# Optimization experiments

Hardware: AMD Instinct MI355X
Metric: run time of the kernel (lower is better)

The kernel has to match this reference:

```python
import jax, jax.numpy as jnp
import numpy as np

N_NODES = 100000


def gcn_conv(x, src, dst, W, b, n):
    # PyG GCNConv: add self-loops, symmetric deg^-1/2 normalization,
    # linear transform, gather->scatter-add aggregation, + bias.
    loop = jnp.arange(n, dtype=src.dtype)
    s = jnp.concatenate([src, loop])
    d = jnp.concatenate([dst, loop])
    deg = jax.ops.segment_sum(jnp.ones_like(d, dtype=x.dtype), d, num_segments=n)
    dinv = jnp.where(deg > 0, jax.lax.rsqrt(deg), jnp.zeros_like(deg))
    norm = dinv[s] * dinv[d]            # [E+N]
    h = x @ W                            # [N, out] (transform before propagate)
    msg = h[s] * norm[:, None]           # gather + scale
    out = jax.ops.segment_sum(msg, d, num_segments=n)  # scatter-add to dst
    return out + b


def setup_inputs() -> dict:
    key = jax.random.key(0)
    k = jax.random.split(key, 6)
    n, e, c_in, hid, c_out = N_NODES, 2500000, 5, 32, 1
    x = jax.random.normal(k[0], (n, c_in), dtype=jnp.float32)
    edge_index = jax.random.randint(k[1], (2, e), 0, n, dtype=jnp.int64)
    # Glorot-style init for GCN weights, zero bias (PyG default)
    W1 = jax.random.normal(k[2], (c_in, hid), dtype=jnp.float32) * (1.0 / np.sqrt(c_in))
    b1 = jnp.zeros((hid,), dtype=jnp.float32)
    W2 = jax.random.normal(k[3], (hid, c_out), dtype=jnp.float32) * (1.0 / np.sqrt(hid))
    b2 = jnp.zeros((c_out,), dtype=jnp.float32)
    return {"x": x, "edge_index": edge_index, "W1": W1, "b1": b1, "W2": W2, "b2": b2}


def reference(x, edge_index, W1, b1, W2, b2):
    n = x.shape[0]
    src, dst = edge_index[0], edge_index[1]
    h = jax.nn.relu(gcn_conv(x, src, dst, W1, b1, n))
    # dropout p=0.3 is identity at inference (training=False)
    return jax.nn.sigmoid(gcn_conv(h, src, dst, W2, b2, n))
```

## Files before the change

kernel.cpp:

```cpp
#include <hip/hip_runtime.h>
#include <math.h>


#define NB_SHIFT  8
#define BNODES    256
#define NBK       512
#define CAP       8192
#define CAP_SHIFT 13
#define CHUNK     8192
#define PBLK      512

__global__ void k_init(int* __restrict__ bcur) {
    int b = threadIdx.x;
    if (b < NBK) bcur[b] = b << CAP_SHIFT;
}

__global__ __launch_bounds__(PBLK) void k_part(const int* __restrict__ src,
                                               const int* __restrict__ dst, int E,
                                               int* __restrict__ bcur,
                                               int* __restrict__ pairs) {
    __shared__ int sp[CHUNK];
    __shared__ unsigned short sb[CHUNK];
    __shared__ int cnt[NBK], ofs[NBK], cur[NBK], gbase[NBK];
    int tid = threadIdx.x;
    int base = blockIdx.x * CHUNK;
    int m = min(CHUNK, E - base);

    if (tid < NBK) cnt[tid] = 0;
    __syncthreads();
    for (int i = tid; i < m; i += PBLK)
        atomicAdd(&cnt[dst[base + i] >> NB_SHIFT], 1);
    __syncthreads();
    int v = cnt[tid];
    ofs[tid] = v;
    __syncthreads();
    for (int off = 1; off < NBK; off <<= 1) {
        int u = (tid >= off) ? ofs[tid - off] : 0;
        __syncthreads();
        ofs[tid] += u;
        __syncthreads();
    }
    int pre = ofs[tid] - v;
    ofs[tid] = pre;
    cur[tid] = pre;
    gbase[tid] = v ? atomicAdd(&bcur[tid], v) : 0;
    __syncthreads();
    for (int i = tid; i < m; i += PBLK) {
        int s = src[base + i], d = dst[base + i];
        int b = d >> NB_SHIFT;
        int p = atomicAdd(&cur[b], 1);
        sp[p] = ((d & (BNODES - 1)) << 24) | s;
        sb[p] = (unsigned short)b;
    }
    __syncthreads();
    for (int i = tid; i < m; i += PBLK) {
        int b = sb[i];
        pairs[gbase[b] + (i - ofs[b])] = sp[i];
    }
}

__global__ __launch_bounds__(512) void k_sortb(int* __restrict__ pairs,
                                               const int* __restrict__ bcur,
                                               const float* __restrict__ x,
                                               float* __restrict__ dinv,
                                               float* __restrict__ xs,
                                               int* __restrict__ nofs,
                                               int* __restrict__ deg, int n) {
    __shared__ int stage[CAP];
    __shared__ int stage2[CAP];
    __shared__ int cnt[BNODES], cur[BNODES], scn[BNODES];
    int tid = threadIdx.x;
    int b = blockIdx.x;
    int base = b << CAP_SHIFT;
    int len = min(bcur[b] - base, CAP);

    for (int i = tid; i < len; i += 512) stage[i] = pairs[base + i];
    if (tid < BNODES) cnt[tid] = 0;
    __syncthreads();
    for (int i = tid; i < len; i += 512)
        atomicAdd(&cnt[((unsigned)stage[i]) >> 24], 1);
    __syncthreads();
    int v = (tid < BNODES) ? cnt[tid] : 0;
    if (tid < BNODES) scn[tid] = v;
    __syncthreads();
    for (int off = 1; off < BNODES; off <<= 1) {
        int u = (tid < BNODES && tid >= off) ? scn[tid - off] : 0;
        __syncthreads();
        if (tid < BNODES) scn[tid] += u;
        __syncthreads();
    }
    if (tid < BNODES) {
        int pos = scn[tid] - v;
        cur[tid] = pos;
        int node = (b << NB_SHIFT) + tid;
        if (node < n) {
            nofs[node] = base + pos;
            deg[node] = v;
            float di = rsqrtf((float)v + 1.0f);
            dinv[node] = di;
            const float* xr = x + (size_t)node * 5;
            float* xo = xs + ((size_t)node << 3);
#pragma unroll
            for (int k = 0; k < 5; ++k) xo[k] = xr[k] * di;
        }
    }
    __syncthreads();
    for (int i = tid; i < len; i += 512) {
        int vv = stage[i];
        int p = atomicAdd(&cur[((unsigned)vv) >> 24], 1);
        stage2[p] = vv & 0x00FFFFFF;
    }
    __syncthreads();
    for (int i = tid; i < len; i += 512) pairs[base + i] = stage2[i];
}

__global__ __launch_bounds__(256) void k_agg1(const int* __restrict__ pairs,
                                              const int* __restrict__ nofs,
                                              const int* __restrict__ deg,
                                              const float* __restrict__ xs,
                                              const float* __restrict__ dinv,
                                              const float* __restrict__ W1,
                                              const float* __restrict__ b1,
                                              const float* __restrict__ W2,
                                              float* __restrict__ h2s, int n) {
    __shared__ float w1[160], bb1[32], w2[32];
    int tid = threadIdx.x;
    if (tid < 160) w1[tid] = W1[tid];
    else if (tid < 192) bb1[tid - 160] = b1[tid - 160];
    else if (tid < 224) w2[tid - 192] = W2[tid - 192];
    __syncthreads();
    int node = blockIdx.x * 128 + (tid >> 1);
    int half = tid & 1;
    if (node >= n) return;
    int beg = nofs[node], dg = deg[node];
    float a0 = 0.f, a1 = 0.f, a2 = 0.f, a3 = 0.f, a4 = 0.f;
    if (!half) {
        const float* xo = xs + ((size_t)node << 3);
        a0 = xo[0]; a1 = xo[1]; a2 = xo[2]; a3 = xo[3]; a4 = xo[4];
    }
    for (int e = beg + half; e < beg + dg; e += 2) {
        int s = pairs[e];
        const float* xr = xs + ((size_t)s << 3);
        float4 q = *(const float4*)xr;
        float q4 = xr[4];
        a0 += q.x; a1 += q.y; a2 += q.z; a3 += q.w; a4 += q4;
    }
    a0 += __shfl_xor(a0, 1); a1 += __shfl_xor(a1, 1); a2 += __shfl_xor(a2, 1);
    a3 += __shfl_xor(a3, 1); a4 += __shfl_xor(a4, 1);
    if (half) return;
    float di = dinv[node];
    a0 *= di; a1 *= di; a2 *= di; a3 *= di; a4 *= di;
    float sum = 0.f;
#pragma unroll
    for (int c = 0; c < 32; ++c) {
        float z = bb1[c] + a0 * w1[c] + a1 * w1[32 + c] + a2 * w1[64 + c]
                         + a3 * w1[96 + c] + a4 * w1[128 + c];
        sum += fmaxf(z, 0.f) * w2[c];
    }
    h2s[node] = sum * di;
}

__global__ __launch_bounds__(256) void k_agg2(const int* __restrict__ pairs,
                                              const int* __restrict__ nofs,
                                              const int* __restrict__ deg,
                                              const float* __restrict__ h2s,
                                              const float* __restrict__ dinv,
                                              const float* __restrict__ b2,
                                              float* __restrict__ out, int n) {
    int tid = threadIdx.x;
    int node = blockIdx.x * 128 + (tid >> 1);
    int half = tid & 1;
    if (node >= n) return;
    int beg = nofs[node], dg = deg[node];
    float a = 0.f;
    for (int e = beg + half; e < beg + dg; e += 2) a += h2s[pairs[e]];
    a += __shfl_xor(a, 1);
    if (half) return;
    float v = dinv[node] * (a + h2s[node]) + b2[0];
    out[node] = 1.0f / (1.0f + __expf(-v));
}

extern "C" void kernel_launch(void* const* d_in, const int* in_sizes, int n_in,
                              void* d_out, int out_size, void* d_ws, size_t ws_size,
                              hipStream_t stream) {
    const float* x  = (const float*)d_in[0];
    const int*   ei = (const int*)d_in[1];
    const float* W1 = (const float*)d_in[2];
    const float* b1 = (const float*)d_in[3];
    const float* W2 = (const float*)d_in[4];
    const float* b2 = (const float*)d_in[5];
    float* out = (float*)d_out;

    const int n = in_sizes[0] / 5;
    const int E = in_sizes[1] / 2;
    const int* src = ei;
    const int* dst = ei + E;
    const int nb = (n + BNODES - 1) >> NB_SHIFT;

    int* wsi = (int*)d_ws;
    int*   pairs = wsi;
    int*   nofs  = wsi + ((size_t)(nb + 1) << CAP_SHIFT);
    int*   deg   = nofs + n;
    float* dinv  = (float*)(deg + n);
    float* h2s   = dinv + n;
    float* xs    = h2s + n;
    int*   bcur  = (int*)(xs + (size_t)8 * n);

    const int nchunk = (E + CHUNK - 1) / CHUNK;
    const int nagg   = (n + 127) / 128;

    k_init<<<1, NBK, 0, stream>>>(bcur);
    k_part<<<nchunk, PBLK, 0, stream>>>(src, dst, E, bcur, pairs);
    k_sortb<<<nb, 512, 0, stream>>>(pairs, bcur, x, dinv, xs, nofs, deg, n);
    k_agg1<<<nagg, 256, 0, stream>>>(pairs, nofs, deg, xs, dinv, W1, b1, W2, h2s, n);
    k_agg2<<<nagg, 256, 0, stream>>>(pairs, nofs, deg, h2s, dinv, b2, out, n);
}
```

Measured before the change: 156.8 us.

## Split bucket sort into count pass and fuse scatter with layer-1 aggregation

The per-bucket sort is split in two. A first kernel only counts per-node degrees and writes dinv and scaled features. A second kernel redoes the scatter into shared memory, writes the sorted pairs back, and immediately runs layer-1 aggregation from shared memory, with 512 threads covering one bucket's 256 nodes. This removes the separate agg1 pass over global pairs and the shared-memory staging copy, at the cost of reading pairs twice and running aggregation with one block per bucket (fewer, larger blocks). CHUNK in the partition kernel is also reduced, which gives more partition blocks.

```diff
diff --git a/kernel.cpp b/kernel.cpp
--- a/kernel.cpp
+++ b/kernel.cpp
@@ -7,7 +7,7 @@
 #define NBK       512
 #define CAP       8192
 #define CAP_SHIFT 13
-#define CHUNK     8192
+#define CHUNK     4888
 #define PBLK      512
 
 __global__ void k_init(int* __restrict__ bcur) {
@@ -59,26 +59,23 @@
     }
 }
 
-__global__ __launch_bounds__(512) void k_sortb(int* __restrict__ pairs,
+__global__ __launch_bounds__(512) void k_sorta(const int* __restrict__ pairs,
                                                const int* __restrict__ bcur,
                                                const float* __restrict__ x,
                                                float* __restrict__ dinv,
                                                float* __restrict__ xs,
                                                int* __restrict__ nofs,
                                                int* __restrict__ deg, int n) {
-    __shared__ int stage[CAP];
-    __shared__ int stage2[CAP];
-    __shared__ int cnt[BNODES], cur[BNODES], scn[BNODES];
+    __shared__ int cnt[BNODES], scn[BNODES];
     int tid = threadIdx.x;
     int b = blockIdx.x;
     int base = b << CAP_SHIFT;
     int len = min(bcur[b] - base, CAP);
 
-    for (int i = tid; i < len; i += 512) stage[i] = pairs[base + i];
     if (tid < BNODES) cnt[tid] = 0;
     __syncthreads();
     for (int i = tid; i < len; i += 512)
-        atomicAdd(&cnt[((unsigned)stage[i]) >> 24], 1);
+        atomicAdd(&cnt[((unsigned)pairs[base + i]) >> 24], 1);
     __syncthreads();
     int v = (tid < BNODES) ? cnt[tid] : 0;
     if (tid < BNODES) scn[tid] = v;
@@ -90,11 +87,9 @@
         __syncthreads();
     }
     if (tid < BNODES) {
-        int pos = scn[tid] - v;
-        cur[tid] = pos;
         int node = (b << NB_SHIFT) + tid;
         if (node < n) {
-            nofs[node] = base + pos;
+            nofs[node] = base + scn[tid] - v;
             deg[node] = v;
             float di = rsqrtf((float)v + 1.0f);
             dinv[node] = di;
@@ -104,42 +99,55 @@
             for (int k = 0; k < 5; ++k) xo[k] = xr[k] * di;
         }
     }
-    __syncthreads();
-    for (int i = tid; i < len; i += 512) {
-        int vv = stage[i];
-        int p = atomicAdd(&cur[((unsigned)vv) >> 24], 1);
-        stage2[p] = vv & 0x00FFFFFF;
-    }
-    __syncthreads();
-    for (int i = tid; i < len; i += 512) pairs[base + i] = stage2[i];
-}
-
-__global__ __launch_bounds__(256) void k_agg1(const int* __restrict__ pairs,
-                                              const int* __restrict__ nofs,
-                                              const int* __restrict__ deg,
-                                              const float* __restrict__ xs,
-                                              const float* __restrict__ dinv,
-                                              const float* __restrict__ W1,
-                                              const float* __restrict__ b1,
-                                              const float* __restrict__ W2,
-                                              float* __restrict__ h2s, int n) {
+}
+
+__global__ __launch_bounds__(512) void k_sortagg1(int* __restrict__ pairs,
+                                                  const int* __restrict__ bcur,
+                                                  const int* __restrict__ nofs,
+                                                  const int* __restrict__ deg,
+                                                  const float* __restrict__ xs,
+                                                  const float* __restrict__ dinv,
+                                                  const float* __restrict__ W1,
+                                                  const float* __restrict__ b1,
+                                                  const float* __restrict__ W2,
+                                                  float* __restrict__ h2s, int n) {
+    __shared__ int stage2[CAP];
+    __shared__ int ofs[BNODES], cnt[BNODES], cur[BNODES];
     __shared__ float w1[160], bb1[32], w2[32];
     int tid = threadIdx.x;
+    int b = blockIdx.x;
+    int nbase = b << NB_SHIFT;
+    int base = b << CAP_SHIFT;
+    int len = min(bcur[b] - base, CAP);
+
     if (tid < 160) w1[tid] = W1[tid];
     else if (tid < 192) bb1[tid - 160] = b1[tid - 160];
     else if (tid < 224) w2[tid - 192] = W2[tid - 192];
-    __syncthreads();
-    int node = blockIdx.x * 128 + (tid >> 1);
-    int half = tid & 1;
+    if (tid < BNODES) {
+        int node = nbase + tid;
+        int o = 0, c = 0;
+        if (node < n) { o = nofs[node] - base; c = deg[node]; }
+        ofs[tid] = o; cnt[tid] = c; cur[tid] = o;
+    }
+    __syncthreads();
+    for (int i = tid; i < len; i += 512) {
+        int vv = pairs[base + i];
+        int p = atomicAdd(&cur[((unsigned)vv) >> 24], 1);
+        stage2[p] = vv & 0x00FFFFFF;
+    }
+    __syncthreads();
+    for (int i = tid; i < len; i += 512) pairs[base + i] = stage2[i];
+    int t2 = tid >> 1, half = tid & 1;
+    int node = nbase + t2;
     if (node >= n) return;
-    int beg = nofs[node], dg = deg[node];
+    int beg = ofs[t2], dg = cnt[t2];
     float a0 = 0.f, a1 = 0.f, a2 = 0.f, a3 = 0.f, a4 = 0.f;
     if (!half) {
         const float* xo = xs + ((size_t)node << 3);
         a0 = xo[0]; a1 = xo[1]; a2 = xo[2]; a3 = xo[3]; a4 = xo[4];
     }
     for (int e = beg + half; e < beg + dg; e += 2) {
-        int s = pairs[e];
+        int s = stage2[e];
         const float* xr = xs + ((size_t)s << 3);
         float4 q = *(const float4*)xr;
         float q4 = xr[4];
@@ -211,7 +219,8 @@
 
     k_init<<<1, NBK, 0, stream>>>(bcur);
     k_part<<<nchunk, PBLK, 0, stream>>>(src, dst, E, bcur, pairs);
-    k_sortb<<<nb, 512, 0, stream>>>(pairs, bcur, x, dinv, xs, nofs, deg, n);
-    k_agg1<<<nagg, 256, 0, stream>>>(pairs, nofs, deg, xs, dinv, W1, b1, W2, h2s, n);
+    k_sorta<<<nb, 512, 0, stream>>>(pairs, bcur, x, dinv, xs, nofs, deg, n);
+    k_sortagg1<<<nb, 512, 0, stream>>>(pairs, bcur, nofs, deg, xs, dinv,
+                                       W1, b1, W2, h2s, n);
     k_agg2<<<nagg, 256, 0, stream>>>(pairs, nofs, deg, h2s, dinv, b2, out, n);
 }
```

New measurement: 146.5 us. 6.6% less time.
